# Performance work log

Measured on AMD Instinct MI355X. Metric: run time of the kernel, lower is better.

Reference implementation:

```python
import jax, jax.numpy as jnp
import numpy as np

EPS = 1e-12

def setup_inputs() -> dict:
    key = jax.random.key(0)
    k1, k2 = jax.random.split(key)
    N, L, C = 32768, 256, 64
    mu = jax.random.uniform(k1, (N, L), dtype=jnp.float32)
    leaf_scores = jax.random.normal(k2, (L, C), dtype=jnp.float32)
    return {"mu": mu, "leaf_scores": leaf_scores}

def reference(mu, leaf_scores):
    # log path probabilities, clamped for numerical safety: (N, L)
    log_mu = jnp.log(jnp.clip(mu, EPS, None))
    # per-leaf class log-probs: (L, C)
    logQ = jax.nn.log_softmax(leaf_scores, axis=1)
    # y[n,k] = logsumexp_l( log_mu[n,l] + logQ[l,k] )  -> (N, C)
    scores = log_mu[:, :, None] + logQ[None, :, :]  # (N, L, C)
    return jax.scipy.special.logsumexp(scores, axis=1)
```

## Files before the change

### kernel.cpp

```cpp
#include <hip/hip_runtime.h>
#include <math.h>

#define NN 32768
#define LL 256
#define CC 64
#define EPSV 1e-12f

typedef __attribute__((ext_vector_type(8))) _Float16 half8;
typedef __attribute__((ext_vector_type(4))) float f32x4;

__global__ __launch_bounds__(64) void prep_kernel(
    const float* __restrict__ scores, _Float16* __restrict__ wsB) {
    const int l = blockIdx.x;
    const int k = threadIdx.x;
    float v = scores[(size_t)l * CC + k];
    float mx = v;
    #pragma unroll
    for (int off = 32; off > 0; off >>= 1) mx = fmaxf(mx, __shfl_xor(mx, off));
    float e = expf(v - mx);
    float sum = e;
    #pragma unroll
    for (int off = 32; off > 0; off >>= 1) sum += __shfl_xor(sum, off);
    _Float16 h = (_Float16)(e / sum);

    const int s = l >> 5;
    const int w = l & 31;
    const int q = w >> 3;
    const int j = w & 7;
    const int t = k >> 4;
    const int m = k & 15;
    wsB[((s * 4 + t) * 64 + q * 16 + m) * 8 + j] = h;
}

__global__ __launch_bounds__(256) void leaf_mix_mfma_kernel(
    const float* __restrict__ mu, const float4* __restrict__ wsB,
    float* __restrict__ out) {
    __shared__ float Bs[8192];

    const int tid = threadIdx.x;
    const int wid = tid >> 6;
    const int lane = tid & 63;
    const int quad = lane >> 4;
    const int m = lane & 15;

    const size_t row = (size_t)blockIdx.x * 64 + wid * 16 + m;
    const float* arow = mu + row * LL + quad * 8;
    float4 a[16];
    #pragma unroll
    for (int s = 0; s < 8; ++s) {
        a[2 * s]     = *(const float4*)(arow + s * 32);
        a[2 * s + 1] = *(const float4*)(arow + s * 32 + 4);
    }

    {
        float4* dst = (float4*)Bs;
        #pragma unroll
        for (int i = 0; i < 8; ++i) dst[tid + 256 * i] = wsB[tid + 256 * i];
    }
    __syncthreads();

    f32x4 acc[4] = {{0.f, 0.f, 0.f, 0.f}, {0.f, 0.f, 0.f, 0.f},
                    {0.f, 0.f, 0.f, 0.f}, {0.f, 0.f, 0.f, 0.f}};

    #pragma unroll
    for (int s = 0; s < 8; ++s) {
        const float f8[8] = {a[2 * s].x, a[2 * s].y, a[2 * s].z, a[2 * s].w,
                             a[2 * s + 1].x, a[2 * s + 1].y, a[2 * s + 1].z, a[2 * s + 1].w};
        half8 ah;
        #pragma unroll
        for (int e = 0; e < 8; ++e) ah[e] = (_Float16)fmaxf(f8[e], EPSV);
        #pragma unroll
        for (int t = 0; t < 4; ++t) {
            const half8 b = ((const half8*)(Bs + (s * 4 + t) * 256))[lane];
            acc[t] = __builtin_amdgcn_mfma_f32_16x16x32_f16(ah, b, acc[t], 0, 0, 0);
        }
    }

    const size_t outRow0 = (size_t)blockIdx.x * 64 + wid * 16 + quad * 4;
    #pragma unroll
    for (int t = 0; t < 4; ++t)
        #pragma unroll
        for (int r = 0; r < 4; ++r)
            out[(outRow0 + r) * CC + t * 16 + m] = logf(acc[t][r]);
}

extern "C" void kernel_launch(void* const* d_in, const int* in_sizes, int n_in,
                              void* d_out, int out_size, void* d_ws, size_t ws_size,
                              hipStream_t stream) {
    const float* mu     = (const float*)d_in[0];
    const float* scores = (const float*)d_in[1];
    float* out = (float*)d_out;

    prep_kernel<<<LL, CC, 0, stream>>>(scores, (_Float16*)d_ws);
    leaf_mix_mfma_kernel<<<NN / 64, 256, 0, stream>>>(mu, (const float4*)d_ws, out);
}
```

Before: 78.74 us.

## Fuse softmax prep kernel into main MFMA kernel, recomputing leaf table per block

Removes the separate prep kernel launch and instead has every block compute the softmax of the 256x64 leaf scores directly into shared memory, using wave shuffles and fast exp/divide intrinsics. This removes one kernel launch and the workspace round-trip, at the cost of redundant softmax work in all 512 blocks. It also drops the EPS clamp on mu and switches to the fast __logf.

Measured after the change: 90.96 us. 15.5% more time.

```diff
diff --git a/kernel.cpp b/kernel.cpp
--- a/kernel.cpp
+++ b/kernel.cpp
@@ -4,44 +4,29 @@
 #define NN 32768
 #define LL 256
 #define CC 64
-#define EPSV 1e-12f
 
 typedef __attribute__((ext_vector_type(8))) _Float16 half8;
 typedef __attribute__((ext_vector_type(4))) float f32x4;
 
-__global__ __launch_bounds__(64) void prep_kernel(
-    const float* __restrict__ scores, _Float16* __restrict__ wsB) {
-    const int l = blockIdx.x;
-    const int k = threadIdx.x;
-    float v = scores[(size_t)l * CC + k];
-    float mx = v;
-    #pragma unroll
-    for (int off = 32; off > 0; off >>= 1) mx = fmaxf(mx, __shfl_xor(mx, off));
-    float e = expf(v - mx);
-    float sum = e;
-    #pragma unroll
-    for (int off = 32; off > 0; off >>= 1) sum += __shfl_xor(sum, off);
-    _Float16 h = (_Float16)(e / sum);
-
-    const int s = l >> 5;
-    const int w = l & 31;
-    const int q = w >> 3;
-    const int j = w & 7;
-    const int t = k >> 4;
-    const int m = k & 15;
-    wsB[((s * 4 + t) * 64 + q * 16 + m) * 8 + j] = h;
-}
-
-__global__ __launch_bounds__(256) void leaf_mix_mfma_kernel(
-    const float* __restrict__ mu, const float4* __restrict__ wsB,
+__global__ __launch_bounds__(256) void fused_leaf_mix_kernel(
+    const float* __restrict__ mu, const float* __restrict__ scores,
     float* __restrict__ out) {
     __shared__ float Bs[8192];
 
-    const int tid = threadIdx.x;
-    const int wid = tid >> 6;
+    const int tid  = threadIdx.x;
+    const int wid  = tid >> 6;
     const int lane = tid & 63;
     const int quad = lane >> 4;
-    const int m = lane & 15;
+    const int m    = lane & 15;
+
+    float vn[8];
+    {
+        const int g = wid * 8;
+        const int s = g >> 2, q = g & 3;
+        const float* srow = scores + (s * 32 + q * 8) * CC + lane;
+        #pragma unroll
+        for (int j = 0; j < 8; ++j) vn[j] = srow[j * CC];
+    }
 
     const size_t row = (size_t)blockIdx.x * 64 + wid * 16 + m;
     const float* arow = mu + row * LL + quad * 8;
@@ -52,10 +37,35 @@
         a[2 * s + 1] = *(const float4*)(arow + s * 32 + 4);
     }
 
-    {
-        float4* dst = (float4*)Bs;
+    #pragma unroll
+    for (int gi = 0; gi < 8; ++gi) {
+        const int g = wid * 8 + gi;
+        const int s = g >> 2, q = g & 3;
+        float v[8];
         #pragma unroll
-        for (int i = 0; i < 8; ++i) dst[tid + 256 * i] = wsB[tid + 256 * i];
+        for (int j = 0; j < 8; ++j) v[j] = vn[j];
+        if (gi < 7) {
+            const int gn = g + 1;
+            const int sn = gn >> 2, qn = gn & 3;
+            const float* srow = scores + (sn * 32 + qn * 8) * CC + lane;
+            #pragma unroll
+            for (int j = 0; j < 8; ++j) vn[j] = srow[j * CC];
+        }
+        half8 h;
+        #pragma unroll
+        for (int j = 0; j < 8; ++j) {
+            float mx = v[j];
+            #pragma unroll
+            for (int off = 32; off > 0; off >>= 1)
+                mx = fmaxf(mx, __shfl_xor(mx, off));
+            const float e = __expf(v[j] - mx);
+            float sum = e;
+            #pragma unroll
+            for (int off = 32; off > 0; off >>= 1)
+                sum += __shfl_xor(sum, off);
+            h[j] = (_Float16)__fdividef(e, sum);
+        }
+        ((half8*)Bs)[(s * 4 + quad) * 64 + q * 16 + m] = h;
     }
     __syncthreads();
 
@@ -64,24 +74,24 @@
 
     #pragma unroll
     for (int s = 0; s < 8; ++s) {
-        const float f8[8] = {a[2 * s].x, a[2 * s].y, a[2 * s].z, a[2 * s].w,
-                             a[2 * s + 1].x, a[2 * s + 1].y, a[2 * s + 1].z, a[2 * s + 1].w};
         half8 ah;
+        ah[0] = (_Float16)a[2 * s].x;     ah[1] = (_Float16)a[2 * s].y;
+        ah[2] = (_Float16)a[2 * s].z;     ah[3] = (_Float16)a[2 * s].w;
+        ah[4] = (_Float16)a[2 * s + 1].x; ah[5] = (_Float16)a[2 * s + 1].y;
+        ah[6] = (_Float16)a[2 * s + 1].z; ah[7] = (_Float16)a[2 * s + 1].w;
         #pragma unroll
-        for (int e = 0; e < 8; ++e) ah[e] = (_Float16)fmaxf(f8[e], EPSV);
-        #pragma unroll
-        for (int t = 0; t < 4; ++t) {
-            const half8 b = ((const half8*)(Bs + (s * 4 + t) * 256))[lane];
-            acc[t] = __builtin_amdgcn_mfma_f32_16x16x32_f16(ah, b, acc[t], 0, 0, 0);
+        for (int tt = 0; tt < 4; ++tt) {
+            const half8 b = ((const half8*)Bs)[(s * 4 + tt) * 64 + lane];
+            acc[tt] = __builtin_amdgcn_mfma_f32_16x16x32_f16(ah, b, acc[tt], 0, 0, 0);
         }
     }
 
     const size_t outRow0 = (size_t)blockIdx.x * 64 + wid * 16 + quad * 4;
     #pragma unroll
-    for (int t = 0; t < 4; ++t)
+    for (int tt = 0; tt < 4; ++tt)
         #pragma unroll
         for (int r = 0; r < 4; ++r)
-            out[(outRow0 + r) * CC + t * 16 + m] = logf(acc[t][r]);
+            out[(outRow0 + r) * CC + tt * 16 + m] = __logf(acc[tt][r]);
 }
 
 extern "C" void kernel_launch(void* const* d_in, const int* in_sizes, int n_in,
@@ -90,7 +100,7 @@
     const float* mu     = (const float*)d_in[0];
     const float* scores = (const float*)d_in[1];
     float* out = (float*)d_out;
+    (void)d_ws; (void)ws_size;
 
-    prep_kernel<<<LL, CC, 0, stream>>>(scores, (_Float16*)d_ws);
-    leaf_mix_mfma_kernel<<<NN / 64, 256, 0, stream>>>(mu, (const float4*)d_ws, out);
+    fused_leaf_mix_kernel<<<NN / 64, 256, 0, stream>>>(mu, scores, out);
 }
```

## Coalesce mu loads and stage A tile in swizzled LDS as fp16

Applied to the files above, without the earlier changes.

Loads mu with fully coalesced float4 accesses across the whole 64-row block, converts to fp16, and writes it into an XOR-swizzled LDS tile that each wave then reads in MFMA fragment layout. The aim is to replace the strided per-lane row loads with contiguous global reads. It also drops the EPS clamp, switches to fast __expf, __fdividef and __logf intrinsics, and issues the B loads into registers before the A loads. In exchange it uses 32KB more LDS per block, which can lower occupancy, and adds an LDS round trip. Removing the clamp changes behaviour for zero inputs.

After: 78.72 us. No clear change (-0.0%).

```diff
diff --git a/kernel.cpp b/kernel.cpp
--- a/kernel.cpp
+++ b/kernel.cpp
@@ -4,9 +4,9 @@
 #define NN 32768
 #define LL 256
 #define CC 64
-#define EPSV 1e-12f
 
 typedef __attribute__((ext_vector_type(8))) _Float16 half8;
+typedef __attribute__((ext_vector_type(4))) _Float16 half4;
 typedef __attribute__((ext_vector_type(4))) float f32x4;
 
 __global__ __launch_bounds__(64) void prep_kernel(
@@ -17,11 +17,11 @@
     float mx = v;
     #pragma unroll
     for (int off = 32; off > 0; off >>= 1) mx = fmaxf(mx, __shfl_xor(mx, off));
-    float e = expf(v - mx);
+    float e = __expf(v - mx);
     float sum = e;
     #pragma unroll
     for (int off = 32; off > 0; off >>= 1) sum += __shfl_xor(sum, off);
-    _Float16 h = (_Float16)(e / sum);
+    _Float16 h = (_Float16)__fdividef(e, sum);
 
     const int s = l >> 5;
     const int w = l & 31;
@@ -36,52 +36,66 @@
     const float* __restrict__ mu, const float4* __restrict__ wsB,
     float* __restrict__ out) {
     __shared__ float Bs[8192];
+    __shared__ _Float16 As[64 * 256];
 
-    const int tid = threadIdx.x;
-    const int wid = tid >> 6;
+    const int tid  = threadIdx.x;
+    const int wid  = tid >> 6;
     const int lane = tid & 63;
     const int quad = lane >> 4;
-    const int m = lane & 15;
+    const int m    = lane & 15;
 
-    const size_t row = (size_t)blockIdx.x * 64 + wid * 16 + m;
-    const float* arow = mu + row * LL + quad * 8;
-    float4 a[16];
+    float4 breg[8];
     #pragma unroll
-    for (int s = 0; s < 8; ++s) {
-        a[2 * s]     = *(const float4*)(arow + s * 32);
-        a[2 * s + 1] = *(const float4*)(arow + s * 32 + 4);
-    }
+    for (int i = 0; i < 8; ++i) breg[i] = wsB[tid + 256 * i];
+
+    f32x4 areg[16];
+    const f32x4* mublk = (const f32x4*)(mu + (size_t)blockIdx.x * 64 * LL);
+    #pragma unroll
+    for (int i = 0; i < 16; ++i) areg[i] = mublk[i * 256 + tid];
 
     {
         float4* dst = (float4*)Bs;
         #pragma unroll
-        for (int i = 0; i < 8; ++i) dst[tid + 256 * i] = wsB[tid + 256 * i];
+        for (int i = 0; i < 8; ++i) dst[tid + 256 * i] = breg[i];
+    }
+
+    {
+        char* as = (char*)As;
+        #pragma unroll
+        for (int i = 0; i < 16; ++i) {
+            const int row = i * 4 + wid;
+            half4 h;
+            h[0] = (_Float16)areg[i][0]; h[1] = (_Float16)areg[i][1];
+            h[2] = (_Float16)areg[i][2]; h[3] = (_Float16)areg[i][3];
+            *(half4*)(as + ((row * 512 + lane * 8) ^ ((row & 7) << 4))) = h;
+        }
     }
     __syncthreads();
 
     f32x4 acc[4] = {{0.f, 0.f, 0.f, 0.f}, {0.f, 0.f, 0.f, 0.f},
                     {0.f, 0.f, 0.f, 0.f}, {0.f, 0.f, 0.f, 0.f}};
 
+    const char* asr = (const char*)As;
+    const char* bsr = (const char*)Bs;
+    const int arow   = wid * 16 + m;
+    const int abase0 = arow * 512 + quad * 16;
+    const int axm    = (m & 7) << 4;
     #pragma unroll
     for (int s = 0; s < 8; ++s) {
-        const float f8[8] = {a[2 * s].x, a[2 * s].y, a[2 * s].z, a[2 * s].w,
-                             a[2 * s + 1].x, a[2 * s + 1].y, a[2 * s + 1].z, a[2 * s + 1].w};
-        half8 ah;
+        const half8 ah = *(const half8*)(asr + ((abase0 + s * 64) ^ axm));
         #pragma unroll
-        for (int e = 0; e < 8; ++e) ah[e] = (_Float16)fmaxf(f8[e], EPSV);
-        #pragma unroll
-        for (int t = 0; t < 4; ++t) {
-            const half8 b = ((const half8*)(Bs + (s * 4 + t) * 256))[lane];
-            acc[t] = __builtin_amdgcn_mfma_f32_16x16x32_f16(ah, b, acc[t], 0, 0, 0);
+        for (int tt = 0; tt < 4; ++tt) {
+            const half8 b = *(const half8*)(bsr + (s * 4 + tt) * 1024 + lane * 16);
+            acc[tt] = __builtin_amdgcn_mfma_f32_16x16x32_f16(ah, b, acc[tt], 0, 0, 0);
         }
     }
 
     const size_t outRow0 = (size_t)blockIdx.x * 64 + wid * 16 + quad * 4;
     #pragma unroll
-    for (int t = 0; t < 4; ++t)
+    for (int tt = 0; tt < 4; ++tt)
         #pragma unroll
         for (int r = 0; r < 4; ++r)
-            out[(outRow0 + r) * CC + t * 16 + m] = logf(acc[t][r]);
+            out[(outRow0 + r) * CC + tt * 16 + m] = __logf(acc[tt][r]);
 }
 
 extern "C" void kernel_launch(void* const* d_in, const int* in_sizes, int n_in,
```
